# Kernel tuning notes

Measured on AMD Instinct MI355X. Metric: run time of the kernel, lower is better.

## Reference

```python
import jax, jax.numpy as jnp
import numpy as np

T_TEXT, T_VIS, T_AUD = 512, 512, 512
BSZ, EMBED, HEADS = 8, 1024, 16


def setup_inputs() -> dict:
    key = jax.random.key(0)
    k1, k2, k3 = jax.random.split(key, 3)
    T = T_TEXT + T_VIS + T_AUD
    # xavier-uniform-like scales
    s_in = float(np.sqrt(6.0 / (3 * EMBED + EMBED)))
    s_out = float(np.sqrt(6.0 / (2 * EMBED)))
    return {
        "x": jax.random.normal(k1, (T, BSZ, EMBED), jnp.float32),
        "in_proj_w": jax.random.uniform(k2, (3 * EMBED, EMBED), jnp.float32, -s_in, s_in),
        "in_proj_b": jnp.zeros((3 * EMBED,), jnp.float32),
        "out_w": jax.random.uniform(k3, (EMBED, EMBED), jnp.float32, -s_out, s_out),
        "out_b": jnp.zeros((EMBED,), jnp.float32),
        "text_len": T_TEXT,
        "vision_len": T_VIS,
        "audio_len": T_AUD,
    }


def reference(x, in_proj_w, in_proj_b, out_w, out_b, text_len, vision_len, audio_len):
    # x: (T, B, E), time-major as in the torch module
    tgt_len, bsz, E = x.shape
    H = HEADS
    d = E // H
    # fused in-projection (qkv_same path), torch F.linear: x @ W^T + b
    qkv = jnp.einsum('tbe,fe->tbf', x, in_proj_w) + in_proj_b  # (T,B,3E)
    q, k, v = jnp.split(qkv, 3, axis=-1)
    q = q * (d ** -0.5)

    def to_bh(t):  # (T,B,E) -> (B*H, T, d)
        return t.reshape(tgt_len, bsz * H, d).transpose(1, 0, 2)

    q, k, v = to_bh(q), to_bh(k), to_bh(v)

    seg = [(0, text_len),
           (text_len, text_len + vision_len),
           (text_len + vision_len, text_len + vision_len + audio_len)]
    # direction == 'forward': text attends vision, vision attends audio, audio attends text
    pairs = [(0, 1), (1, 2), (2, 0)]

    outs = []
    for qi, ki in pairs:
        qa = q[:, seg[qi][0]:seg[qi][1]]  # (BH, Tq, d)
        kb = k[:, seg[ki][0]:seg[ki][1]]  # (BH, Tk, d)
        vb = v[:, seg[ki][0]:seg[ki][1]]  # (BH, Tk, d)
        w = jax.nn.softmax(jnp.einsum('btd,bsd->bts', qa, kb), axis=-1)
        outs.append(jnp.einsum('bts,bsd->btd', w, vb))

    attn = jnp.concatenate(outs, axis=1)  # (BH, T, d)
    attn = attn.transpose(1, 0, 2).reshape(tgt_len, bsz, E)
    return jnp.einsum('tbe,fe->tbf', attn, out_w) + out_b
```

## Files before the change

### kernel.cpp

```cpp
#include <hip/hip_runtime.h>
#include <hip/hip_bf16.h>


#define T_ALL 1536
#define BSZ 8
#define EMBED 1024
#define HEADS 16
#define HDIM 64
#define SEG 512
#define PLANE 12582912ull
#define QSCALE 0.180336880f

using bf16 = __hip_bfloat16;
using ushort = unsigned short;
typedef __attribute__((ext_vector_type(8))) short bf16x8;
typedef __attribute__((ext_vector_type(4))) float f32x4;
typedef __attribute__((ext_vector_type(8))) unsigned short ushort8;

__device__ inline float bf2f(ushort u) {
  return __uint_as_float(((unsigned int)u) << 16);
}
__device__ inline ushort f2bf(float f) {
  unsigned int x = __float_as_uint(f);
  x += 0x7fffu + ((x >> 16) & 1u);
  return (ushort)(x >> 16);
}

#define GLOAD_LDS16(g, l)                                      \
  __builtin_amdgcn_global_load_lds(                            \
      (const __attribute__((address_space(1))) void*)(g),      \
      (__attribute__((address_space(3))) void*)(l), 16, 0, 0)

__global__ __launch_bounds__(256) void cast3_bf16(
    const float* __restrict__ x, const float* __restrict__ w_in,
    const float* __restrict__ w_out, ushort* __restrict__ xb,
    ushort* __restrict__ w_inb, ushort* __restrict__ w_outb) {
  int i4 = blockIdx.x * 256 + threadIdx.x;
  const float* src;
  ushort* dst;
  if (i4 < 3145728) {
    src = x; dst = xb;
  } else if (i4 < 3145728 + 786432) {
    i4 -= 3145728; src = w_in; dst = w_inb;
  } else {
    i4 -= 3145728 + 786432; src = w_out; dst = w_outb;
  }
  float4 v = *(const float4*)(src + (size_t)i4 * 4);
  ushort4 u;
  u.x = f2bf(v.x); u.y = f2bf(v.y); u.z = f2bf(v.z); u.w = f2bf(v.w);
  *(ushort4*)(dst + (size_t)i4 * 4) = u;
}

#define BAR_LGKM()                                     \
  __builtin_amdgcn_s_barrier();                        \
  asm volatile("s_waitcnt lgkmcnt(0)" ::: "memory");   \
  __builtin_amdgcn_sched_barrier(0);

#define MFMA24(J0)                                                         \
  __builtin_amdgcn_s_setprio(1);                                           \
  _Pragma("unroll")                                                        \
  for (int i = 0; i < 6; ++i) {                                            \
    _Pragma("unroll")                                                      \
    for (int j = J0; j < J0 + 2; ++j) {                                    \
      acc[i][j] = __builtin_amdgcn_mfma_f32_16x16x32_bf16(                 \
          af[i][0], bf[j][0], acc[i][j], 0, 0, 0);                         \
      acc[i][j] = __builtin_amdgcn_mfma_f32_16x16x32_bf16(                 \
          af[i][1], bf[j][1], acc[i][j], 0, 0, 0);                         \
    }                                                                      \
  }                                                                        \
  __builtin_amdgcn_s_setprio(0);

template <typename TC, bool PLANAR>
__global__ __launch_bounds__(512, 2) void gemm192_nt(
    const ushort* __restrict__ A, const ushort* __restrict__ B,
    const float* __restrict__ bias, TC* __restrict__ C,
    int N, int K, int nN) {
  __shared__ char lds[114688];
  const int tid = threadIdx.x;
  const int lane = tid & 63, wid = tid >> 6;
  const int wr = wid >> 2, wcn = wid & 3;
  const int r16 = lane & 15, g4 = lane >> 4;

  const int nwg = gridDim.x;
  const int bid = blockIdx.x;
  const int swz = (bid & 7) * (nwg >> 3) + (bid >> 3);
  const int m0 = (swz / nN) * 192, n0 = (swz % nN) * 256;

  const int NT = K >> 6;

  auto STAGE_A = [&](int ldso, int kcol) {
#pragma unroll
    for (int q = 0; q < 3; ++q) {
      int row = q * 64 + (tid >> 3);
      int sl = (tid & 7) ^ (row & 7);
      const ushort* src = A + (size_t)(m0 + row) * K + kcol + sl * 8;
      GLOAD_LDS16(src, lds + ldso + row * 128 + (tid & 7) * 16);
    }
  };
  auto STAGE_B = [&](int gr0, int ldso, int kcol) {
#pragma unroll
    for (int q = 0; q < 2; ++q) {
      int row = q * 64 + (tid >> 3);
      int sl = (tid & 7) ^ (row & 7);
      const ushort* src = B + (size_t)(gr0 + row) * K + kcol + sl * 8;
      GLOAD_LDS16(src, lds + ldso + row * 128 + (tid & 7) * 16);
    }
  };
  auto LD = [&](int ldso, int row, int kk) -> bf16x8 {
    return *(const bf16x8*)(lds + ldso + row * 128 +
                            ((kk * 64 + g4 * 16) ^ ((row & 7) << 4)));
  };

  f32x4 acc[6][4];
#pragma unroll
  for (int i = 0; i < 6; ++i)
#pragma unroll
    for (int j = 0; j < 4; ++j) acc[i][j] = f32x4{0.f, 0.f, 0.f, 0.f};

  STAGE_A(0, 0);
  STAGE_B(n0, 24576, 0);
  STAGE_B(n0 + 128, 24576 + 16384, 0);
  asm volatile("s_waitcnt vmcnt(0)" ::: "memory");
  __builtin_amdgcn_s_barrier();

  bf16x8 af[6][2], bf[4][2];
  int cur = 0;
  for (int t = 0; t < NT; ++t) {
    const int aC = cur * 57344, bC = aC + 24576;
    const int aN = (cur ^ 1) * 57344, bN = aN + 24576;
#pragma unroll
    for (int i = 0; i < 6; ++i) {
      int ar = wr * 96 + i * 16 + r16;
      af[i][0] = LD(aC, ar, 0);
      af[i][1] = LD(aC, ar, 1);
    }
#pragma unroll
    for (int j = 0; j < 2; ++j) {
      int br = wcn * 32 + j * 16 + r16;
      bf[j][0] = LD(bC, br, 0);
      bf[j][1] = LD(bC, br, 1);
    }
    if (t + 1 < NT) {
      STAGE_A(aN, (t + 1) * 64);
      STAGE_B(n0, bN, (t + 1) * 64);
    }
    BAR_LGKM();
    MFMA24(0);
    __builtin_amdgcn_s_barrier();
    if (t + 1 < NT)
      asm volatile("s_waitcnt vmcnt(5)" ::: "memory");
    else
      asm volatile("s_waitcnt vmcnt(0)" ::: "memory");
    __builtin_amdgcn_s_barrier();
#pragma unroll
    for (int j = 2; j < 4; ++j) {
      int br = wcn * 32 + 128 + (j & 1) * 16 + r16;
      bf[j][0] = LD(bC, br, 0);
      bf[j][1] = LD(bC, br, 1);
    }
    if (t + 1 < NT) STAGE_B(n0 + 128, bN + 16384, (t + 1) * 64);
    BAR_LGKM();
    MFMA24(2);
    __builtin_amdgcn_s_barrier();
    if (t + 1 < NT) {
      asm volatile("s_waitcnt vmcnt(2)" ::: "memory");
      __builtin_amdgcn_s_barrier();
    }
    cur ^= 1;
  }

#pragma unroll
  for (int i = 0; i < 6; ++i) {
    int row = m0 + wr * 96 + i * 16 + g4 * 4;
#pragma unroll
    for (int j = 0; j < 4; ++j) {
      int col = n0 + wcn * 32 + (j >> 1) * 128 + (j & 1) * 16 + r16;
      float bs = bias[col];
      if constexpr (PLANAR) {
        const int which = col >> 10;
        const int ch = col & 1023;
        const int h = ch >> 6, d = ch & 63;
        const float scl = (which == 0) ? QSCALE : 1.f;
#pragma unroll
        for (int r = 0; r < 4; ++r) {
          int rr = row + r;
          int tt = rr >> 3, b = rr & 7;
          float v = (acc[i][j][r] + bs) * scl;
          ((ushort*)C)[(size_t)which * PLANE +
                       (((size_t)(b * 16 + h) * 1536 + tt) << 6) + d] = f2bf(v);
        }
      } else {
#pragma unroll
        for (int r = 0; r < 4; ++r) {
          float v = acc[i][j][r] + bs;
          if constexpr (sizeof(TC) == 2)
            ((ushort*)C)[(size_t)(row + r) * N + col] = f2bf(v);
          else
            ((float*)C)[(size_t)(row + r) * N + col] = v;
        }
      }
    }
  }
}

__global__ __launch_bounds__(256) void attn_mfma(
    const ushort* __restrict__ qkv,
    ushort* __restrict__ attn) {
  __shared__ ushort Vt[64 * 64];
  __shared__ ushort Ps[128 * 64];
  const int qt = blockIdx.x;
  const int pr = blockIdx.y;
  const int bh = blockIdx.z;
  const int b = bh >> 4, h = bh & 15;
  const int t = threadIdx.x;
  const int lane = t & 63, w = t >> 6;
  const int r16 = lane & 15;
  const int g4 = lane >> 4;
  const int q_t0 = pr * SEG + qt * 128;
  const int k_t0 = ((pr + 1) % 3) * SEG;

  const ushort* qb = qkv + (size_t)bh * 1536 * 64;
  const ushort* kb = qb + PLANE;
  const ushort* vb = qb + 2 * PLANE;

  bf16x8 qf[2][2];
#pragma unroll
  for (int i = 0; i < 2; ++i)
#pragma unroll
    for (int ks = 0; ks < 2; ++ks)
      qf[i][ks] = *(const bf16x8*)(qb +
          (size_t)(q_t0 + w * 32 + i * 16 + r16) * 64 + ks * 32 + g4 * 8);

  f32x4 acc[2][4];
  float lsum[2][4];
#pragma unroll
  for (int i = 0; i < 2; ++i) {
#pragma unroll
    for (int j = 0; j < 4; ++j) acc[i][j] = f32x4{0.f, 0.f, 0.f, 0.f};
#pragma unroll
    for (int r = 0; r < 4; ++r) lsum[i][r] = 0.f;
  }

  const int vd0 = w * 16;
  bf16x8 kf[2][4][2];
  ushort8 vv[2][2];
#pragma unroll
  for (int j = 0; j < 4; ++j)
#pragma unroll
    for (int ks = 0; ks < 2; ++ks)
      kf[0][j][ks] = *(const bf16x8*)(kb +
          (size_t)(k_t0 + j * 16 + r16) * 64 + ks * 32 + g4 * 8);
  {
    const ushort* vsrc = vb + (size_t)(k_t0 + lane) * 64 + vd0;
    vv[0][0] = *(const ushort8*)vsrc;
    vv[0][1] = *(const ushort8*)(vsrc + 8);
  }

#pragma unroll
  for (int sc8 = 0; sc8 < 8; ++sc8) {
    const int cur = sc8 & 1, nxt = cur ^ 1;

    f32x4 s4[2][4];
#pragma unroll
    for (int i = 0; i < 2; ++i)
#pragma unroll
      for (int j = 0; j < 4; ++j) {
        f32x4 a = f32x4{0.f, 0.f, 0.f, 0.f};
        a = __builtin_amdgcn_mfma_f32_16x16x32_bf16(qf[i][0], kf[cur][j][0], a, 0, 0, 0);
        a = __builtin_amdgcn_mfma_f32_16x16x32_bf16(qf[i][1], kf[cur][j][1], a, 0, 0, 0);
        s4[i][j] = a;
      }

    if (sc8 < 7) {
      const int s_n = k_t0 + (sc8 + 1) * 64;
#pragma unroll
      for (int j = 0; j < 4; ++j)
#pragma unroll
        for (int ks = 0; ks < 2; ++ks)
          kf[nxt][j][ks] = *(const bf16x8*)(kb +
              (size_t)(s_n + j * 16 + r16) * 64 + ks * 32 + g4 * 8);
      const ushort* vsrc = vb + (size_t)(s_n + lane) * 64 + vd0;
      vv[nxt][0] = *(const ushort8*)vsrc;
      vv[nxt][1] = *(const ushort8*)(vsrc + 8);
    }

#pragma unroll
    for (int i = 0; i < 2; ++i)
#pragma unroll
      for (int r = 0; r < 4; ++r) {
        float rs = 0.f;
#pragma unroll
        for (int j = 0; j < 4; ++j) {
          float p = __builtin_amdgcn_exp2f(s4[i][j][r]);
          s4[i][j][r] = p;
          rs += p;
        }
        lsum[i][r] += rs;
      }

    __syncthreads();

#pragma unroll
    for (int jj = 0; jj < 16; ++jj) {
      int d = vd0 + jj;
      ushort val = (jj < 8) ? vv[cur][0][jj] : vv[cur][1][jj - 8];
      *(ushort*)((char*)Vt + d * 128 + ((lane * 2) ^ ((d & 7) << 4))) = val;
    }
#pragma unroll
    for (int i = 0; i < 2; ++i)
#pragma unroll
      for (int j = 0; j < 4; ++j)
#pragma unroll
        for (int r = 0; r < 4; ++r) {
          int ql = w * 32 + i * 16 + g4 * 4 + r;
          int sl = j * 16 + r16;
          *(ushort*)((char*)Ps + ql * 128 +
                     ((sl * 2) ^ ((ql & 7) << 4))) = f2bf(s4[i][j][r]);
        }
    __syncthreads();

    bf16x8 pa[2][2], vbf[4][2];
#pragma unroll
    for (int i = 0; i < 2; ++i)
#pragma unroll
      for (int ks = 0; ks < 2; ++ks) {
        int ql = w * 32 + i * 16 + r16;
        pa[i][ks] = *(bf16x8*)((char*)Ps + ql * 128 +
                               ((ks * 64 + g4 * 16) ^ ((ql & 7) << 4)));
      }
#pragma unroll
    for (int j = 0; j < 4; ++j)
#pragma unroll
      for (int ks = 0; ks < 2; ++ks) {
        int d = j * 16 + r16;
        vbf[j][ks] = *(bf16x8*)((char*)Vt + d * 128 +
                                ((ks * 64 + g4 * 16) ^ ((d & 7) << 4)));
      }
#pragma unroll
    for (int i = 0; i < 2; ++i)
#pragma unroll
      for (int j = 0; j < 4; ++j) {
        acc[i][j] = __builtin_amdgcn_mfma_f32_16x16x32_bf16(pa[i][0], vbf[j][0],
                                                            acc[i][j], 0, 0, 0);
        acc[i][j] = __builtin_amdgcn_mfma_f32_16x16x32_bf16(pa[i][1], vbf[j][1],
                                                            acc[i][j], 0, 0, 0);
      }
  }

#pragma unroll
  for (int i = 0; i < 2; ++i)
#pragma unroll
    for (int r = 0; r < 4; ++r) {
      float rs = lsum[i][r];
      rs += __shfl_xor(rs, 1);
      rs += __shfl_xor(rs, 2);
      rs += __shfl_xor(rs, 4);
      rs += __shfl_xor(rs, 8);
      float inv = 1.f / rs;
      int tq = q_t0 + w * 32 + i * 16 + g4 * 4 + r;
      size_t base = ((size_t)tq * BSZ + b) * 1024 + h * 64;
#pragma unroll
      for (int j = 0; j < 4; ++j)
        attn[base + j * 16 + r16] = f2bf(acc[i][j][r] * inv);
    }
}

extern "C" void kernel_launch(void* const* d_in, const int* in_sizes, int n_in,
                              void* d_out, int out_size, void* d_ws,
                              size_t ws_size, hipStream_t stream) {
  const float* x     = (const float*)d_in[0];
  const float* w_in  = (const float*)d_in[1];
  const float* b_in  = (const float*)d_in[2];
  const float* w_out = (const float*)d_in[3];
  const float* b_out = (const float*)d_in[4];

  char* ws = (char*)d_ws;
  ushort* xb     = (ushort*)ws;
  ushort* w_inb  = (ushort*)(ws + 25165824ull);
  ushort* qkv    = (ushort*)(ws + 31457280ull);
  ushort* w_outb = (ushort*)(ws + 106954752ull);
  ushort* attn   = (ushort*)ws;

  cast3_bf16<<<16384, 256, 0, stream>>>(x, w_in, w_out, xb, w_inb, w_outb);

  gemm192_nt<ushort, true><<<768, 512, 0, stream>>>(
      xb, w_inb, b_in, qkv, 3072, 1024, 12);

  attn_mfma<<<dim3(4, 3, 128), 256, 0, stream>>>(qkv, attn);

  gemm192_nt<float, false><<<256, 512, 0, stream>>>(
      attn, w_outb, b_out, (float*)d_out, 1024, 1024, 4);
}
```

Before: 229.3 us.

## Double-buffer attention LDS tiles to drop one barrier per key chunk

The attention kernel now double-buffers its shared-memory P and V tiles, so each 64-key chunk needs one barrier instead of two. The explicit register prefetch of the next K/V chunk is removed in favour of in-loop loads, and launch bounds request 3 blocks per CU. The grid is reordered so consecutive blocks cover different batch-heads rather than different query tiles of the same head. This trades higher LDS use (double buffers) and loss of software prefetch for fewer barriers and possibly higher occupancy.

```diff
diff --git a/kernel.cpp b/kernel.cpp
--- a/kernel.cpp
+++ b/kernel.cpp
@@ -203,14 +203,14 @@
   }
 }
 
-__global__ __launch_bounds__(256) void attn_mfma(
+__global__ __launch_bounds__(256, 3) void attn_mfma(
     const ushort* __restrict__ qkv,
     ushort* __restrict__ attn) {
-  __shared__ ushort Vt[64 * 64];
-  __shared__ ushort Ps[128 * 64];
-  const int qt = blockIdx.x;
+  __shared__ ushort Vt[2][64 * 64];
+  __shared__ ushort Ps[2][128 * 64];
+  const int bh = blockIdx.x;
   const int pr = blockIdx.y;
-  const int bh = blockIdx.z;
+  const int qt = blockIdx.z;
   const int b = bh >> 4, h = bh & 15;
   const int t = threadIdx.x;
   const int lane = t & 63, w = t >> 6;
@@ -242,23 +242,22 @@
   }
 
   const int vd0 = w * 16;
-  bf16x8 kf[2][4][2];
-  ushort8 vv[2][2];
-#pragma unroll
-  for (int j = 0; j < 4; ++j)
-#pragma unroll
-    for (int ks = 0; ks < 2; ++ks)
-      kf[0][j][ks] = *(const bf16x8*)(kb +
-          (size_t)(k_t0 + j * 16 + r16) * 64 + ks * 32 + g4 * 8);
-  {
-    const ushort* vsrc = vb + (size_t)(k_t0 + lane) * 64 + vd0;
-    vv[0][0] = *(const ushort8*)vsrc;
-    vv[0][1] = *(const ushort8*)(vsrc + 8);
-  }
 
 #pragma unroll
   for (int sc8 = 0; sc8 < 8; ++sc8) {
-    const int cur = sc8 & 1, nxt = cur ^ 1;
+    const int cur = sc8 & 1;
+    const int s0 = k_t0 + sc8 * 64;
+
+    bf16x8 kf[4][2];
+#pragma unroll
+    for (int j = 0; j < 4; ++j)
+#pragma unroll
+      for (int ks = 0; ks < 2; ++ks)
+        kf[j][ks] = *(const bf16x8*)(kb +
+            (size_t)(s0 + j * 16 + r16) * 64 + ks * 32 + g4 * 8);
+    const ushort* vsrc = vb + (size_t)(s0 + lane) * 64 + vd0;
+    ushort8 v0 = *(const ushort8*)vsrc;
+    ushort8 v1 = *(const ushort8*)(vsrc + 8);
 
     f32x4 s4[2][4];
 #pragma unroll
@@ -266,23 +265,10 @@
 #pragma unroll
       for (int j = 0; j < 4; ++j) {
         f32x4 a = f32x4{0.f, 0.f, 0.f, 0.f};
-        a = __builtin_amdgcn_mfma_f32_16x16x32_bf16(qf[i][0], kf[cur][j][0], a, 0, 0, 0);
-        a = __builtin_amdgcn_mfma_f32_16x16x32_bf16(qf[i][1], kf[cur][j][1], a, 0, 0, 0);
+        a = __builtin_amdgcn_mfma_f32_16x16x32_bf16(qf[i][0], kf[j][0], a, 0, 0, 0);
+        a = __builtin_amdgcn_mfma_f32_16x16x32_bf16(qf[i][1], kf[j][1], a, 0, 0, 0);
         s4[i][j] = a;
       }
-
-    if (sc8 < 7) {
-      const int s_n = k_t0 + (sc8 + 1) * 64;
-#pragma unroll
-      for (int j = 0; j < 4; ++j)
-#pragma unroll
-        for (int ks = 0; ks < 2; ++ks)
-          kf[nxt][j][ks] = *(const bf16x8*)(kb +
-              (size_t)(s_n + j * 16 + r16) * 64 + ks * 32 + g4 * 8);
-      const ushort* vsrc = vb + (size_t)(s_n + lane) * 64 + vd0;
-      vv[nxt][0] = *(const ushort8*)vsrc;
-      vv[nxt][1] = *(const ushort8*)(vsrc + 8);
-    }
 
 #pragma unroll
     for (int i = 0; i < 2; ++i)
@@ -298,13 +284,11 @@
         lsum[i][r] += rs;
       }
 
-    __syncthreads();
-
 #pragma unroll
     for (int jj = 0; jj < 16; ++jj) {
       int d = vd0 + jj;
-      ushort val = (jj < 8) ? vv[cur][0][jj] : vv[cur][1][jj - 8];
-      *(ushort*)((char*)Vt + d * 128 + ((lane * 2) ^ ((d & 7) << 4))) = val;
+      ushort val = (jj < 8) ? v0[jj] : v1[jj - 8];
+      *(ushort*)((char*)Vt[cur] + d * 128 + ((lane * 2) ^ ((d & 7) << 4))) = val;
     }
 #pragma unroll
     for (int i = 0; i < 2; ++i)
@@ -314,10 +298,14 @@
         for (int r = 0; r < 4; ++r) {
           int ql = w * 32 + i * 16 + g4 * 4 + r;
           int sl = j * 16 + r16;
-          *(ushort*)((char*)Ps + ql * 128 +
+          *(ushort*)((char*)Ps[cur] + ql * 128 +
                      ((sl * 2) ^ ((ql & 7) << 4))) = f2bf(s4[i][j][r]);
         }
-    __syncthreads();
+
+    asm volatile("s_waitcnt lgkmcnt(0)" ::: "memory");
+    __builtin_amdgcn_sched_barrier(0);
+    __builtin_amdgcn_s_barrier();
+    __builtin_amdgcn_sched_barrier(0);
 
     bf16x8 pa[2][2], vbf[4][2];
 #pragma unroll
@@ -325,7 +313,7 @@
 #pragma unroll
       for (int ks = 0; ks < 2; ++ks) {
         int ql = w * 32 + i * 16 + r16;
-        pa[i][ks] = *(bf16x8*)((char*)Ps + ql * 128 +
+        pa[i][ks] = *(bf16x8*)((char*)Ps[cur] + ql * 128 +
                                ((ks * 64 + g4 * 16) ^ ((ql & 7) << 4)));
       }
 #pragma unroll
@@ -333,7 +321,7 @@
 #pragma unroll
       for (int ks = 0; ks < 2; ++ks) {
         int d = j * 16 + r16;
-        vbf[j][ks] = *(bf16x8*)((char*)Vt + d * 128 +
+        vbf[j][ks] = *(bf16x8*)((char*)Vt[cur] + d * 128 +
                                 ((ks * 64 + g4 * 16) ^ ((d & 7) << 4)));
       }
 #pragma unroll
@@ -386,7 +374,7 @@
   gemm192_nt<ushort, true><<<768, 512, 0, stream>>>(
       xb, w_inb, b_in, qkv, 3072, 1024, 12);
 
-  attn_mfma<<<dim3(4, 3, 128), 256, 0, stream>>>(qkv, attn);
+  attn_mfma<<<dim3(128, 3, 4), 256, 0, stream>>>(qkv, attn);
 
   gemm192_nt<float, false><<<256, 512, 0, stream>>>(
       attn, w_outb, b_out, (float*)d_out, 1024, 1024, 4);
```

After: 200.6 us. 1.14x faster.
